# Kernel optimization log

Hardware: AMD Instinct MI355X
Metric: run time of the kernel (lower is better)

The kernel has to match this reference:

```python
import jax, jax.numpy as jnp
import numpy as np

NUM_UNIQUE = 256     # number of distinct edge types (static)
STRENGTH = 0.01      # regularizer strength (init kwarg)


def setup_inputs() -> dict:
    key = jax.random.key(0)
    k1, k2, k3 = jax.random.split(key, 3)
    E = 33554432  # 2^25 synapses
    x = jax.random.normal(k1, (E,), dtype=jnp.float32)
    idx = jax.random.randint(k2, (E,), 0, NUM_UNIQUE, dtype=jnp.int32)
    target_mean = jax.random.normal(k3, (NUM_UNIQUE,), dtype=jnp.float32)
    return {"x": x, "idx": idx, "target_mean": target_mean}


def reference(x, idx, target_mean):
    # unsorted_segment_mean: scatter-add of values and counts per edge type
    seg_sum = jax.ops.segment_sum(x, idx, num_segments=NUM_UNIQUE)
    seg_cnt = jax.ops.segment_sum(jnp.ones_like(x), idx, num_segments=NUM_UNIQUE)
    mean_w = seg_sum / jnp.maximum(seg_cnt, 1.0)  # TF yields 0 for empty segments
    dev = mean_w - target_mean
    reg_loss = jnp.mean(jnp.square(dev))
    return reg_loss * jnp.float32(STRENGTH)
```

## Files before the change

kernel.cpp:

```cpp
#include <hip/hip_runtime.h>
#include <hip/hip_bf16.h>

#define NBINS 256
#define NCOPIES 4
#define STRENGTH 0.01f

#define CNT_SHIFT 41
#define FP_SCALE 524288.0f
#define FP_INV_SCALE (1.0 / 524288.0)
#define FP_BIAS (1 << 23)

__device__ __forceinline__ unsigned long long pack_elem(float x) {
    int v = __float2int_rn(x * FP_SCALE) + FP_BIAS;
    v = min(max(v, 0), (1 << 24) - 1);
    return (1ULL << CNT_SHIFT) | (unsigned long long)(unsigned int)v;
}

__global__ __launch_bounds__(1024) void seg_hist_kernel(
    const float4* __restrict__ x4,
    const int4* __restrict__ idx4,
    float* __restrict__ gsum,
    unsigned int* __restrict__ gcnt,
    int nvec)
{
    __shared__ unsigned long long h[NCOPIES][NBINS];

    for (int i = threadIdx.x; i < NCOPIES * NBINS; i += blockDim.x)
        ((unsigned long long*)h)[i] = 0ull;
    __syncthreads();

    unsigned long long* hist = h[(threadIdx.x >> 6) & (NCOPIES - 1)];

    const int stride = gridDim.x * blockDim.x;
    for (int i = blockIdx.x * blockDim.x + threadIdx.x; i < nvec; i += stride) {
        const float4 xv = x4[i];
        const int4  iv = idx4[i];
        atomicAdd(&hist[iv.x], pack_elem(xv.x));
        atomicAdd(&hist[iv.y], pack_elem(xv.y));
        atomicAdd(&hist[iv.z], pack_elem(xv.z));
        atomicAdd(&hist[iv.w], pack_elem(xv.w));
    }
    __syncthreads();

    for (int b = threadIdx.x; b < NBINS; b += blockDim.x) {
        unsigned long long p = h[0][b] + h[1][b] + h[2][b] + h[3][b];
        unsigned int cnt = (unsigned int)(p >> CNT_SHIFT);
        long long lowsum = (long long)(p & ((1ULL << CNT_SHIFT) - 1))
                         - (long long)cnt * FP_BIAS;
        if (cnt) {
            float s = (float)((double)lowsum * FP_INV_SCALE);
            atomicAdd(&gsum[b], s);
            atomicAdd(&gcnt[b], cnt);
        }
    }
}

__global__ __launch_bounds__(NBINS) void finalize_kernel(
    const float* __restrict__ gsum,
    const unsigned int* __restrict__ gcnt,
    const float* __restrict__ target,
    float* __restrict__ out)
{
    const int t = threadIdx.x;
    const float s = gsum[t];
    const float c = (float)gcnt[t];
    const float mean = s / fmaxf(c, 1.0f);
    const float dev = mean - target[t];
    float v = dev * dev;

    #pragma unroll
    for (int off = 32; off > 0; off >>= 1) {
        v += __shfl_down(v, off, 64);
    }
    __shared__ float red[4];
    if ((t & 63) == 0) red[t >> 6] = v;
    __syncthreads();
    if (t == 0) {
        const float tot = red[0] + red[1] + red[2] + red[3];
        out[0] = tot * (STRENGTH / (float)NBINS);
    }
}

extern "C" void kernel_launch(void* const* d_in, const int* in_sizes, int n_in,
                              void* d_out, int out_size, void* d_ws, size_t ws_size,
                              hipStream_t stream)
{
    const float* x      = (const float*)d_in[0];
    const int*   idx    = (const int*)d_in[1];
    const float* target = (const float*)d_in[2];
    float*       out    = (float*)d_out;

    const int E    = in_sizes[0];
    const int nvec = E / 4;

    float*        gsum = (float*)d_ws;
    unsigned int* gcnt = (unsigned int*)(gsum + NBINS);

    hipMemsetAsync(d_ws, 0, NBINS * (sizeof(float) + sizeof(unsigned int)), stream);

    const int block = 1024;
    const int grid  = 512;
    seg_hist_kernel<<<grid, block, 0, stream>>>(
        (const float4*)x, (const int4*)idx, gsum, gcnt, nvec);

    finalize_kernel<<<1, NBINS, 0, stream>>>(gsum, gcnt, target, out);
}
```

Before: 280.4 us.

## Split histogram atomics between per-wave LDS copies and global per-block regions

Half of each thread's four elements now go to a private per-wave LDS histogram and the other half to a global 64-bit histogram region chosen by block index. The goal is to spread atomic throughput across both LDS and the L2 atomic units, and to remove LDS contention by giving every wave its own copy. Blocks shrink to 512 threads while the grid doubles. The finalize kernel folds in 512 region histograms serially per bin, and the memset now clears about 1 MB. Both of those add serial cost, and the global atomics are shared by two blocks per region.

New measurement: 648.1 us. +131.1%, slower.

```diff
diff --git a/kernel.cpp b/kernel.cpp
--- a/kernel.cpp
+++ b/kernel.cpp
@@ -2,7 +2,8 @@
 #include <hip/hip_bf16.h>
 
 #define NBINS 256
-#define NCOPIES 4
+#define NREG 512
+#define NWAVES 8
 #define STRENGTH 0.01f
 
 #define CNT_SHIFT 41
@@ -16,20 +17,22 @@
     return (1ULL << CNT_SHIFT) | (unsigned long long)(unsigned int)v;
 }
 
-__global__ __launch_bounds__(1024) void seg_hist_kernel(
+__global__ __launch_bounds__(512) void seg_hist_kernel(
     const float4* __restrict__ x4,
     const int4* __restrict__ idx4,
     float* __restrict__ gsum,
     unsigned int* __restrict__ gcnt,
+    unsigned long long* __restrict__ regions,
     int nvec)
 {
-    __shared__ unsigned long long h[NCOPIES][NBINS];
+    __shared__ unsigned long long h[NWAVES][NBINS];
 
-    for (int i = threadIdx.x; i < NCOPIES * NBINS; i += blockDim.x)
+    for (int i = threadIdx.x; i < NWAVES * NBINS; i += blockDim.x)
         ((unsigned long long*)h)[i] = 0ull;
     __syncthreads();
 
-    unsigned long long* hist = h[(threadIdx.x >> 6) & (NCOPIES - 1)];
+    unsigned long long* hist = h[threadIdx.x >> 6];
+    unsigned long long* reg  = regions + (unsigned)(blockIdx.x & (NREG - 1)) * NBINS;
 
     const int stride = gridDim.x * blockDim.x;
     for (int i = blockIdx.x * blockDim.x + threadIdx.x; i < nvec; i += stride) {
@@ -37,19 +40,20 @@
         const int4  iv = idx4[i];
         atomicAdd(&hist[iv.x], pack_elem(xv.x));
         atomicAdd(&hist[iv.y], pack_elem(xv.y));
-        atomicAdd(&hist[iv.z], pack_elem(xv.z));
-        atomicAdd(&hist[iv.w], pack_elem(xv.w));
+        atomicAdd(&reg[iv.z], pack_elem(xv.z));
+        atomicAdd(&reg[iv.w], pack_elem(xv.w));
     }
     __syncthreads();
 
     for (int b = threadIdx.x; b < NBINS; b += blockDim.x) {
-        unsigned long long p = h[0][b] + h[1][b] + h[2][b] + h[3][b];
+        unsigned long long p = 0ull;
+        #pragma unroll
+        for (int w = 0; w < NWAVES; ++w) p += h[w][b];
         unsigned int cnt = (unsigned int)(p >> CNT_SHIFT);
-        long long lowsum = (long long)(p & ((1ULL << CNT_SHIFT) - 1))
-                         - (long long)cnt * FP_BIAS;
         if (cnt) {
-            float s = (float)((double)lowsum * FP_INV_SCALE);
-            atomicAdd(&gsum[b], s);
+            long long lowsum = (long long)(p & ((1ULL << CNT_SHIFT) - 1))
+                             - (long long)cnt * FP_BIAS;
+            atomicAdd(&gsum[b], (float)((double)lowsum * FP_INV_SCALE));
             atomicAdd(&gcnt[b], cnt);
         }
     }
@@ -58,14 +62,24 @@
 __global__ __launch_bounds__(NBINS) void finalize_kernel(
     const float* __restrict__ gsum,
     const unsigned int* __restrict__ gcnt,
+    const unsigned long long* __restrict__ regions,
     const float* __restrict__ target,
     float* __restrict__ out)
 {
-    const int t = threadIdx.x;
-    const float s = gsum[t];
-    const float c = (float)gcnt[t];
-    const float mean = s / fmaxf(c, 1.0f);
-    const float dev = mean - target[t];
+    const int b = threadIdx.x;
+
+    long long fix = 0;
+    unsigned long long cnt = 0;
+    for (int r = 0; r < NREG; ++r) {
+        unsigned long long p = regions[(size_t)r * NBINS + b];
+        unsigned long long c = p >> CNT_SHIFT;
+        cnt += c;
+        fix += (long long)(p & ((1ULL << CNT_SHIFT) - 1)) - (long long)c * FP_BIAS;
+    }
+    const double s = (double)gsum[b] + (double)fix * FP_INV_SCALE;
+    const double c_tot = (double)(gcnt[b] + cnt);
+    const float mean = (float)(s / fmax(c_tot, 1.0));
+    const float dev = mean - target[b];
     float v = dev * dev;
 
     #pragma unroll
@@ -73,9 +87,9 @@
         v += __shfl_down(v, off, 64);
     }
     __shared__ float red[4];
-    if ((t & 63) == 0) red[t >> 6] = v;
+    if ((b & 63) == 0) red[b >> 6] = v;
     __syncthreads();
-    if (t == 0) {
+    if (b == 0) {
         const float tot = red[0] + red[1] + red[2] + red[3];
         out[0] = tot * (STRENGTH / (float)NBINS);
     }
@@ -93,15 +107,17 @@
     const int E    = in_sizes[0];
     const int nvec = E / 4;
 
-    float*        gsum = (float*)d_ws;
-    unsigned int* gcnt = (unsigned int*)(gsum + NBINS);
+    float*              gsum    = (float*)d_ws;
+    unsigned int*       gcnt    = (unsigned int*)(gsum + NBINS);
+    unsigned long long* regions = (unsigned long long*)((char*)d_ws + 4096);
 
-    hipMemsetAsync(d_ws, 0, NBINS * (sizeof(float) + sizeof(unsigned int)), stream);
+    const size_t zero_bytes = 4096 + (size_t)NREG * NBINS * sizeof(unsigned long long);
+    hipMemsetAsync(d_ws, 0, zero_bytes, stream);
 
-    const int block = 1024;
-    const int grid  = 512;
+    const int block = 512;
+    const int grid  = 1024;
     seg_hist_kernel<<<grid, block, 0, stream>>>(
-        (const float4*)x, (const int4*)idx, gsum, gcnt, nvec);
+        (const float4*)x, (const int4*)idx, gsum, gcnt, regions, nvec);
 
-    finalize_kernel<<<1, NBINS, 0, stream>>>(gsum, gcnt, target, out);
+    finalize_kernel<<<1, NBINS, 0, stream>>>(gsum, gcnt, regions, target, out);
 }
```
